# Optimization experiments

Hardware: AMD Instinct MI355X
Metric: run time of the kernel (lower is better)

## Reference

```python
import jax, jax.numpy as jnp
import numpy as np
from jax import lax

B, MID, OUT, H, W = 16, 128, 512, 112, 112
EPS = 1e-5


def _conv(x, w, stride=1, pad=0, dil=1, groups=1):
    return lax.conv_general_dilated(
        x, w, window_strides=(stride, stride),
        padding=[(pad, pad), (pad, pad)], rhs_dilation=(dil, dil),
        feature_group_count=groups,
        dimension_numbers=('NCHW', 'OIHW', 'NCHW'))


def setup_inputs() -> dict:
    key = jax.random.key(0)
    ks = jax.random.split(key, 12)
    s = 0.05
    return {
        'x': jax.random.normal(ks[0], (B, 2 * MID, H, W), jnp.float32),
        # kernel_gen: Linear(mid, mid*9, bias=False) weight [mid*9, mid]
        'W_kg': jax.random.normal(ks[1], (MID * 9, MID), jnp.float32) * s,
        # global stream: depthwise 3x3 dil=2, then 1x1 conv, BN
        'gdw_w': jax.random.normal(ks[2], (MID, 1, 3, 3), jnp.float32) * s,
        'gdw_b': jax.random.normal(ks[3], (MID,), jnp.float32) * s,
        'gpw_w': jax.random.normal(ks[4], (MID, MID, 1, 1), jnp.float32) * s,
        'gpw_b': jax.random.normal(ks[5], (MID,), jnp.float32) * s,
        'bn1_g': jnp.ones((MID,), jnp.float32),
        'bn1_b': jnp.zeros((MID,), jnp.float32),
        'bn1_m': jax.random.normal(ks[6], (MID,), jnp.float32) * s,
        'bn1_v': jax.random.uniform(ks[7], (MID,), jnp.float32, 0.5, 1.5),
        # downsample: Conv2d(2*mid, out, 3, stride=2, pad=1), BN
        'ds_w': jax.random.normal(ks[8], (OUT, 2 * MID, 3, 3), jnp.float32) * s,
        'ds_b': jax.random.normal(ks[9], (OUT,), jnp.float32) * s,
        'bn2_g': jnp.ones((OUT,), jnp.float32),
        'bn2_b': jnp.zeros((OUT,), jnp.float32),
        'bn2_m': jax.random.normal(ks[10], (OUT,), jnp.float32) * s,
        'bn2_v': jax.random.uniform(ks[11], (OUT,), jnp.float32, 0.5, 1.5),
    }


def _bn(x, g, b, m, v):  # eval-mode BatchNorm2d
    inv = g / jnp.sqrt(v + EPS)
    return x * inv[None, :, None, None] + (b - m * inv)[None, :, None, None]


def reference(x, W_kg, gdw_w, gdw_b, gpw_w, gpw_b,
              bn1_g, bn1_b, bn1_m, bn1_v,
              ds_w, ds_b, bn2_g, bn2_b, bn2_m, bn2_v):
    local_in, global_in = jnp.split(x, 2, axis=1)  # [B,MID,H,W] each
    b, c, h, w = local_in.shape

    # local branch: pool -> linear+relu kernel-gen -> per-sample depthwise 3x3
    pooled = jnp.mean(local_in, axis=(2, 3))                  # [b,c]
    kernels = jax.nn.relu(pooled @ W_kg.T)                    # [b, c*9]
    kernels = kernels.reshape(b * c, 1, 3, 3)
    local_out = _conv(local_in.reshape(1, b * c, h, w), kernels,
                      pad=1, groups=b * c).reshape(b, c, h, w)

    # global branch: depthwise dil-2 conv -> 1x1 conv -> BN -> ReLU
    g = _conv(global_in, gdw_w, pad=2, dil=2, groups=c) + gdw_b[None, :, None, None]
    g = _conv(g, gpw_w) + gpw_b[None, :, None, None]
    g = jax.nn.relu(_bn(g, bn1_g, bn1_b, bn1_m, bn1_v))

    combined = jnp.concatenate([local_out, g], axis=1)        # [b,2c,h,w]
    out = _conv(combined, ds_w, stride=2, pad=1) + ds_b[None, :, None, None]
    out = jax.nn.relu(_bn(out, bn2_g, bn2_b, bn2_m, bn2_v))   # [b,OUT,h/2,w/2]
    return out
```

## Files before the change

kernel.cpp:

```cpp
#include <hip/hip_runtime.h>


#define DEVI static __device__ __forceinline__

using bf16x8 = __attribute__((ext_vector_type(8))) short;
using f32x4  = __attribute__((ext_vector_type(4))) float;
typedef unsigned short ushort_t;

constexpr int Bn = 16, MID = 128, CHN = 256, Hh = 112, Wn = 112;
constexpr int OHn = 56, OWn = 56, OCn = 512;
constexpr int HW  = Hh * Wn;
constexpr float EPSf = 1e-5f;

constexpr size_t C_I = 56 * 64;
constexpr size_t C_P = 4 * C_I;
constexpr size_t C_H = 2 * C_P;
constexpr size_t C_B = (size_t)Hh * C_H;

DEVI ushort_t f2b(float f) {
    unsigned u = __float_as_uint(f);
    return (ushort_t)((u + 0x7FFFu + ((u >> 16) & 1u)) >> 16);
}
DEVI float b2f(ushort_t s) { return __uint_as_float(((unsigned)s) << 16); }
DEVI int pack2(float a, float b) {
    return (int)f2b(a) | ((int)f2b(b) << 16);
}

DEVI void gl_lds16(const void* g, void* l) {
    __builtin_amdgcn_global_load_lds(
        (const __attribute__((address_space(1))) unsigned int*)g,
        (__attribute__((address_space(3))) unsigned int*)l, 16, 0, 0);
}

__global__ __launch_bounds__(256) void k_wds(
        const float* __restrict__ dsw, ushort_t* __restrict__ wds2,
        const float* __restrict__ gpw_w, const float* __restrict__ gpw_b,
        const float* __restrict__ bn1g, const float* __restrict__ bn1b,
        const float* __restrict__ bn1m, const float* __restrict__ bn1v,
        const float* __restrict__ dsb,
        const float* __restrict__ bn2g, const float* __restrict__ bn2b,
        const float* __restrict__ bn2m, const float* __restrict__ bn2v,
        ushort_t* __restrict__ gpwbf,
        float* __restrict__ a1, float* __restrict__ b1,
        float* __restrict__ a2, float* __restrict__ b2,
        float* __restrict__ pooled) {
    int d = blockIdx.x * 256 + threadIdx.x;
    int j = d & 63, oc = (d >> 6) & 511, kb = d >> 15;
    int khw = kb >> 2, icc = kb & 3;
    int ph = j >> 3, c = ph ^ (oc & 7);
    int ic = icc * 64 + c * 8 + (j & 7);
    wds2[d] = f2b(dsw[((size_t)oc * CHN + ic) * 9 + khw]);
    int i = d;
    if (i < MID * MID) gpwbf[i] = f2b(gpw_w[i]);
    if (i < Bn * MID) pooled[i] = 0.f;
    if (i < OCn) {
        float inv = bn2g[i] / sqrtf(bn2v[i] + EPSf);
        a2[i] = inv;
        b2[i] = bn2b[i] + (dsb[i] - bn2m[i]) * inv;
    }
    if (i < MID) {
        float inv = bn1g[i] / sqrtf(bn1v[i] + EPSf);
        a1[i] = inv;
        b1[i] = bn1b[i] + (gpw_b[i] - bn1m[i]) * inv;
    }
}

__global__ __launch_bounds__(256) void k_kgen(const float* __restrict__ pooled,
                                              const float* __restrict__ wkg,
                                              float* __restrict__ kgen) {
    int idx = blockIdx.x * 256 + threadIdx.x;
    int b = idx / 1152, j = idx % 1152;
    int c = j & 127, tp = j >> 7;
    const float* pr = pooled + b * MID;
    const float* wr = wkg + (size_t)(c * 9 + tp) * MID;
    float s = 0.f;
#pragma unroll 8
    for (int i = 0; i < MID; i++) s += pr[i] * wr[i];
    kgen[idx] = fmaxf(s * (1.f / HW), 0.f);
}

__global__ __launch_bounds__(256) void k_xt(const float* __restrict__ x,
                                            ushort_t* __restrict__ xT,
                                            float* __restrict__ pooled) {
    __shared__ ushort_t tile[Wn * 264];
    int t = threadIdx.x;
    int bh = blockIdx.x;
    int b = bh / Hh, h = bh % Hh;
    const float* xp = x + ((size_t)b * CHN * Hh + h) * Wn;
    for (int idx = t; idx < CHN * 28; idx += 256) {
        int ch = idx / 28, q = idx % 28;
        float4 v = *(const float4*)(xp + (size_t)ch * HW + q * 4);
        int w = q * 4;
        tile[w * 264 + ch]       = f2b(v.x);
        tile[(w + 1) * 264 + ch] = f2b(v.y);
        tile[(w + 2) * 264 + ch] = f2b(v.z);
        tile[(w + 3) * 264 + ch] = f2b(v.w);
    }
    __syncthreads();
    int4* dst = (int4*)(xT + (size_t)bh * Wn * CHN);
    for (int q = t; q < Wn * CHN / 8; q += 256) {
        int w = q >> 5, c0 = (q & 31) << 3;
        dst[q] = *(const int4*)(tile + w * 264 + c0);
    }
    if (t < MID) {
        float s = 0.f;
        for (int w = 0; w < Wn; w++) s += b2f(tile[w * 264 + t]);
        atomicAdd(&pooled[b * MID + t], s);
    }
}

template <int DIL>
DEVI void dw_accum_row(const ushort_t* __restrict__ rp,
                       const float* __restrict__ wtab, int tb,
                       int c0, int wbase, float (&acc)[7][8]) {
    constexpr int NC = 7 + 2 * DIL;
    float wk[3][8];
#pragma unroll
    for (int dw = 0; dw < 3; dw++) {
        float4 lo = *(const float4*)&wtab[(tb + dw) * 128 + c0];
        float4 hi = *(const float4*)&wtab[(tb + dw) * 128 + c0 + 4];
        wk[dw][0] = lo.x; wk[dw][1] = lo.y; wk[dw][2] = lo.z; wk[dw][3] = lo.w;
        wk[dw][4] = hi.x; wk[dw][5] = hi.y; wk[dw][6] = hi.z; wk[dw][7] = hi.w;
    }
    int4 C[NC];
#pragma unroll
    for (int j = 0; j < NC; j++) {
        int w1 = wbase - DIL + j;
        int4 v = make_int4(0, 0, 0, 0);
        if ((unsigned)w1 < (unsigned)Wn)
            v = *(const int4*)(rp + (size_t)w1 * CHN);
        C[j] = v;
    }
#pragma unroll
    for (int j = 0; j < NC; j++) {
        float f[8];
        {
            unsigned u;
            u = (unsigned)C[j].x;
            f[0] = __uint_as_float(u << 16); f[1] = __uint_as_float(u & 0xffff0000u);
            u = (unsigned)C[j].y;
            f[2] = __uint_as_float(u << 16); f[3] = __uint_as_float(u & 0xffff0000u);
            u = (unsigned)C[j].z;
            f[4] = __uint_as_float(u << 16); f[5] = __uint_as_float(u & 0xffff0000u);
            u = (unsigned)C[j].w;
            f[6] = __uint_as_float(u << 16); f[7] = __uint_as_float(u & 0xffff0000u);
        }
#pragma unroll
        for (int dw = 0; dw < 3; dw++) {
            int i = j - dw * DIL;
            if (i >= 0 && i <= 6) {
#pragma unroll
                for (int k = 0; k < 8; k++) acc[i][k] += wk[dw][k] * f[k];
            }
        }
    }
}

__global__ __launch_bounds__(256, 3) void k_dw(
        const ushort_t* __restrict__ xT, const float* __restrict__ kgen,
        const float* __restrict__ gdw_w, const float* __restrict__ gdw_b,
        ushort_t* __restrict__ comb) {
    __shared__ float wtab[1152];
    int t = threadIdx.x;
    int h = blockIdx.x, by = blockIdx.y;
    int b = by >> 1, br = by & 1;
    if (br == 0) {
        const float4* src = (const float4*)(kgen + (size_t)b * 1152);
        float4* dstw = (float4*)wtab;
        dstw[t] = src[t];
        if (t < 32) dstw[256 + t] = src[256 + t];
    } else {
        for (int e4 = t; e4 < 288; e4 += 256) {
            float4 v = *(const float4*)(gdw_w + (size_t)e4 * 4);
            int e = e4 * 4;
            wtab[(e % 9) * 128 + e / 9]             = v.x;
            wtab[((e + 1) % 9) * 128 + (e + 1) / 9] = v.y;
            wtab[((e + 2) % 9) * 128 + (e + 2) / 9] = v.z;
            wtab[((e + 3) % 9) * 128 + (e + 3) / 9] = v.w;
        }
    }
    __syncthreads();
    int cg = t & 15, wl = t >> 4, c0 = cg << 3, wbase = 7 * wl;
    const ushort_t* xb = xT + (size_t)b * HW * CHN + (br ? MID : 0) + c0;
    float acc[7][8];
    if (br == 0) {
#pragma unroll
        for (int i = 0; i < 7; i++)
#pragma unroll
            for (int k = 0; k < 8; k++) acc[i][k] = 0.f;
#pragma unroll
        for (int dh = -1; dh <= 1; dh++) {
            int h1 = h + dh;
            if ((unsigned)h1 < (unsigned)Hh)
                dw_accum_row<1>(xb + (size_t)h1 * Wn * CHN, wtab,
                                (dh + 1) * 3, c0, wbase, acc);
        }
    } else {
        float4 b0 = *(const float4*)(gdw_b + c0);
        float4 b4 = *(const float4*)(gdw_b + c0 + 4);
#pragma unroll
        for (int i = 0; i < 7; i++) {
            acc[i][0] = b0.x; acc[i][1] = b0.y; acc[i][2] = b0.z; acc[i][3] = b0.w;
            acc[i][4] = b4.x; acc[i][5] = b4.y; acc[i][6] = b4.z; acc[i][7] = b4.w;
        }
#pragma unroll
        for (int dh = -1; dh <= 1; dh++) {
            int h1 = h + 2 * dh;
            if ((unsigned)h1 < (unsigned)Hh)
                dw_accum_row<2>(xb + (size_t)h1 * Wn * CHN, wtab,
                                (dh + 1) * 3, c0, wbase, acc);
        }
    }
    int gch = (br ? MID : 0) + c0;
    int icc = gch >> 6, cch = (gch & 63) >> 3;
#pragma unroll
    for (int i = 0; i < 7; i++) {
        int w = wbase + i;
        int4 O;
        O.x = pack2(acc[i][0], acc[i][1]);
        O.y = pack2(acc[i][2], acc[i][3]);
        O.z = pack2(acc[i][4], acc[i][5]);
        O.w = pack2(acc[i][6], acc[i][7]);
        int w2 = w >> 1, p = w & 1, ph = cch ^ (w2 & 7);
        *(int4*)(comb + (size_t)b * C_B + (size_t)h * C_H + p * C_P
                 + icc * C_I + w2 * 64 + ph * 8) = O;
    }
}

__global__ __launch_bounds__(256, 3) void k_pw(
        ushort_t* __restrict__ comb, const ushort_t* __restrict__ gpwbf,
        const float* __restrict__ a1, const float* __restrict__ b1) {
    __shared__ ushort_t pbuf[112 * 136];
    int t = threadIdx.x, lane = t & 63, wave = t >> 6;
    int h = blockIdx.x, b = blockIdx.y;
    const char* base = (const char*)(comb + (size_t)b * C_B + (size_t)h * C_H);
    for (int j = wave; j < 28; j += 4) {
        int s = j / 7, cc = j - s * 7;
        int p = s >> 1, ic = 2 + (s & 1);
        const char* src = base + ((size_t)p * C_P + (size_t)ic * C_I) * 2
                          + cc * 1024 + lane * 16;
        gl_lds16(src, (char*)pbuf + (size_t)s * 7168 + cc * 1024);
    }
    __syncthreads();
    int mrow = lane & 15, quad = lane >> 4;
    const short* gw = (const short*)gpwbf;
    f32x4 acc2[7][2] = {};
#pragma unroll
    for (int ks = 0; ks < 4; ks++) {
        bf16x8 bfr[2];
#pragma unroll
        for (int n = 0; n < 2; n++)
            bfr[n] = *(const bf16x8*)(gw + (size_t)(wave * 32 + n * 16 + mrow) * MID
                                         + ks * 32 + quad * 8);
        int kq = ks * 4 + quad;
#pragma unroll
        for (int m = 0; m < 7; m++) {
            int row = m * 16 + mrow;
            int p = (row >= 56) ? 1 : 0;
            int w2 = row - 56 * p;
            int slab = p * 2 + (kq >> 3);
            int ph = (kq & 7) ^ (w2 & 7);
            bf16x8 af = *(const bf16x8*)(pbuf + (size_t)slab * 3584
                                         + w2 * 64 + ph * 8);
#pragma unroll
            for (int n = 0; n < 2; n++)
                acc2[m][n] = __builtin_amdgcn_mfma_f32_16x16x32_bf16(
                    af, bfr[n], acc2[m][n], 0, 0, 0);
        }
    }
    __syncthreads();
#pragma unroll
    for (int m = 0; m < 7; m++)
#pragma unroll
        for (int n = 0; n < 2; n++) {
            int oc2 = wave * 32 + n * 16 + mrow;
            float al = a1[oc2], be = b1[oc2];
#pragma unroll
            for (int r = 0; r < 4; r++) {
                int px = m * 16 + quad * 4 + r;
                pbuf[px * 136 + oc2] = f2b(fmaxf(acc2[m][n][r] * al + be, 0.f));
            }
        }
    __syncthreads();
    int cg = t & 15, wl = t >> 4, c0 = cg << 3;
    for (int ws = 0; ws < 7; ws++) {
        int row = ws * 16 + wl;
        int p = (row >= 56) ? 1 : 0;
        int w2 = row - 56 * p;
        int4 v = *(const int4*)(pbuf + (size_t)row * 136 + c0);
        int gch = MID + c0;
        int icc = gch >> 6, cch = (gch & 63) >> 3, ph = cch ^ (w2 & 7);
        *(int4*)(comb + (size_t)b * C_B + (size_t)h * C_H + (size_t)p * C_P
                 + icc * C_I + w2 * 64 + ph * 8) = v;
    }
}

__global__ __launch_bounds__(256) void k_ds(
        const ushort_t* __restrict__ comb, const ushort_t* __restrict__ wds2,
        const float* __restrict__ a2, const float* __restrict__ b2,
        float* __restrict__ out) {
    __shared__ ushort_t lA[128 * 64];
    __shared__ ushort_t lB[128 * 64];
    int t = threadIdx.x, lane = t & 63, wave = t >> 6;
    int g = blockIdx.x;
    int xcd = g & 7, s = g >> 3;
    int octile = s & 3, pl = s >> 2;
    int pair = xcd * 56 + pl;
    int bb = pair / 28, ohp = pair % 28;
    int oh0 = ohp * 2, oc0 = octile * 128;
    int mrow = lane & 15, quad = lane >> 4;
    int wm = wave & 1, wn = wave >> 1;
    int ak = mrow & 7;

    f32x4 acc[4][4] = {};
    for (int kt = 0; kt < 36; kt++) {
        int khw = kt >> 2, icc = kt & 3;
        int kh = khw / 3, kw = khw - kh * 3;
        int p = (kw == 1) ? 0 : 1;
        bool zh0 = (oh0 == 0) && (kh == 0);
        int ldsShift = (kw == 0) ? 128 : 0;
        __syncthreads();
        if (zh0) {
            int4 z = {0, 0, 0, 0};
            *(int4*)(lB + t * 8) = z;
            *(int4*)(lB + 2048 + t * 8) = z;
        }
        if (kw == 0 && t < 16) {
            int4 z = {0, 0, 0, 0};
            *(int4*)(lB + (t >> 3) * 4096 + (t & 7) * 8) = z;
        }
        const char* asrc = (const char*)wds2
            + ((size_t)kt * 32768 + (size_t)oc0 * 64) * 2 + lane * 16;
#pragma unroll
        for (int i = 0; i < 4; i++) {
            int j = wave * 4 + i;
            gl_lds16(asrc + j * 1024, (char*)lA + j * 1024);
        }
        for (int j = wave; j < 14; j += 4) {
            int osub = (j >= 7) ? 1 : 0, jj = j - osub * 7;
            if (zh0 && osub == 0) continue;
            int r = 2 * oh0 + 2 * osub + kh - 1;
            const char* bsrc = (const char*)comb
                + ((size_t)bb * C_B + (size_t)r * C_H + (size_t)p * C_P
                   + (size_t)icc * C_I) * 2 + jj * 1024 + lane * 16;
            gl_lds16(bsrc, (char*)lB + osub * 8192 + ldsShift + jj * 1024);
        }
        __syncthreads();
        int bk = (mrow + ((kw == 0) ? 7 : 0)) & 7;
#pragma unroll
        for (int ks = 0; ks < 2; ks++) {
            bf16x8 af[4], bf[4];
#pragma unroll
            for (int m = 0; m < 4; m++) {
                int row = wm * 64 + m * 16 + mrow;
                int ph = (ks * 4 + quad) ^ ak;
                af[m] = *(const bf16x8*)(lA + row * 64 + ph * 8);
            }
#pragma unroll
            for (int n = 0; n < 4; n++) {
                int nr = wn * 64 + n * 16 + mrow;
                int ph = (ks * 4 + quad) ^ bk;
                bf[n] = *(const bf16x8*)(lB + nr * 64 + ph * 8);
            }
#pragma unroll
            for (int m = 0; m < 4; m++)
#pragma unroll
                for (int n = 0; n < 4; n++)
                    acc[m][n] = __builtin_amdgcn_mfma_f32_16x16x32_bf16(
                        af[m], bf[n], acc[m][n], 0, 0, 0);
        }
    }
#pragma unroll
    for (int m = 0; m < 4; m++) {
#pragma unroll
        for (int r4 = 0; r4 < 4; r4++) {
            int oc = oc0 + wm * 64 + m * 16 + quad * 4 + r4;
            float al = a2[oc], be = b2[oc];
#pragma unroll
            for (int n = 0; n < 4; n++) {
                int nr = wn * 64 + n * 16 + mrow;
                int osub = nr >> 6, ow = nr & 63;
                if (ow < OWn) {
                    float v = fmaxf(acc[m][n][r4] * al + be, 0.f);
                    out[((size_t)(bb * OCn + oc) * OHn + (oh0 + osub)) * OWn + ow] = v;
                }
            }
        }
    }
}

extern "C" void kernel_launch(void* const* d_in, const int* in_sizes, int n_in,
                              void* d_out, int out_size, void* d_ws, size_t ws_size,
                              hipStream_t stream) {
    const float* x     = (const float*)d_in[0];
    const float* wkg   = (const float*)d_in[1];
    const float* gdw_w = (const float*)d_in[2];
    const float* gdw_b = (const float*)d_in[3];
    const float* gpw_w = (const float*)d_in[4];
    const float* gpw_b = (const float*)d_in[5];
    const float* bn1g  = (const float*)d_in[6];
    const float* bn1b  = (const float*)d_in[7];
    const float* bn1m  = (const float*)d_in[8];
    const float* bn1v  = (const float*)d_in[9];
    const float* dsw   = (const float*)d_in[10];
    const float* dsb   = (const float*)d_in[11];
    const float* bn2g  = (const float*)d_in[12];
    const float* bn2b  = (const float*)d_in[13];
    const float* bn2m  = (const float*)d_in[14];
    const float* bn2v  = (const float*)d_in[15];

    char* ws = (char*)d_ws;
    float*    pooled = (float*)(ws + 0);
    float*    kgen   = (float*)(ws + 8192);
    float*    a1     = (float*)(ws + 81920);
    float*    b1     = (float*)(ws + 82432);
    float*    a2     = (float*)(ws + 82944);
    float*    b2     = (float*)(ws + 84992);
    ushort_t* gpwbf  = (ushort_t*)(ws + 87040);
    ushort_t* wds2   = (ushort_t*)(ws + 119808);
    ushort_t* comb   = (ushort_t*)(ws + 2479104);
    ushort_t* xT  = (ushort_t*)d_out;
    float*    out = (float*)d_out;

    k_wds <<<4608, 256, 0, stream>>>(dsw, wds2, gpw_w, gpw_b,
                                     bn1g, bn1b, bn1m, bn1v, dsb,
                                     bn2g, bn2b, bn2m, bn2v,
                                     gpwbf, a1, b1, a2, b2, pooled);
    k_xt  <<<1792, 256, 0, stream>>>(x, xT, pooled);
    k_kgen<<<72, 256, 0, stream>>>(pooled, wkg, kgen);
    k_dw  <<<dim3(Hh, Bn * 2), 256, 0, stream>>>(xT, kgen, gdw_w, gdw_b, comb);
    k_pw  <<<dim3(Hh, Bn), 256, 0, stream>>>(comb, gpwbf, a1, b1);
    k_ds  <<<1792, 256, 0, stream>>>(comb, wds2, a2, b2, out);
}
```

Baseline: 338.8 us.

## Double-buffer LDS tiles in downsample conv GEMM to overlap loads with MFMA

The stride-2 downsample convolution kernel now keeps two LDS buffers for the weight and activation tiles. It issues the global-to-LDS loads for the next K step before running MFMAs on the current one, which halves the barriers per K step and hides load latency behind compute. The cost is doubled LDS use (64KB per block), which may reduce how many blocks fit on a CU.

```diff
diff --git a/kernel.cpp b/kernel.cpp
--- a/kernel.cpp
+++ b/kernel.cpp
@@ -299,8 +299,8 @@
         const ushort_t* __restrict__ comb, const ushort_t* __restrict__ wds2,
         const float* __restrict__ a2, const float* __restrict__ b2,
         float* __restrict__ out) {
-    __shared__ ushort_t lA[128 * 64];
-    __shared__ ushort_t lB[128 * 64];
+    __shared__ __align__(16) ushort_t lA[2][128 * 64];
+    __shared__ __align__(16) ushort_t lB[2][128 * 64];
     int t = threadIdx.x, lane = t & 63, wave = t >> 6;
     int g = blockIdx.x;
     int xcd = g & 7, s = g >> 3;
@@ -312,29 +312,29 @@
     int wm = wave & 1, wn = wave >> 1;
     int ak = mrow & 7;
 
-    f32x4 acc[4][4] = {};
-    for (int kt = 0; kt < 36; kt++) {
+    auto STAGE = [&](int kt, int nb) {
         int khw = kt >> 2, icc = kt & 3;
         int kh = khw / 3, kw = khw - kh * 3;
         int p = (kw == 1) ? 0 : 1;
         bool zh0 = (oh0 == 0) && (kh == 0);
         int ldsShift = (kw == 0) ? 128 : 0;
-        __syncthreads();
+        ushort_t* A = (ushort_t*)lA[nb];
+        ushort_t* B = (ushort_t*)lB[nb];
         if (zh0) {
             int4 z = {0, 0, 0, 0};
-            *(int4*)(lB + t * 8) = z;
-            *(int4*)(lB + 2048 + t * 8) = z;
+            *(int4*)(B + t * 8) = z;
+            *(int4*)(B + 2048 + t * 8) = z;
         }
         if (kw == 0 && t < 16) {
             int4 z = {0, 0, 0, 0};
-            *(int4*)(lB + (t >> 3) * 4096 + (t & 7) * 8) = z;
+            *(int4*)(B + (t >> 3) * 4096 + (t & 7) * 8) = z;
         }
         const char* asrc = (const char*)wds2
             + ((size_t)kt * 32768 + (size_t)oc0 * 64) * 2 + lane * 16;
 #pragma unroll
         for (int i = 0; i < 4; i++) {
             int j = wave * 4 + i;
-            gl_lds16(asrc + j * 1024, (char*)lA + j * 1024);
+            gl_lds16(asrc + j * 1024, (char*)A + j * 1024);
         }
         for (int j = wave; j < 14; j += 4) {
             int osub = (j >= 7) ? 1 : 0, jj = j - osub * 7;
@@ -343,9 +343,16 @@
             const char* bsrc = (const char*)comb
                 + ((size_t)bb * C_B + (size_t)r * C_H + (size_t)p * C_P
                    + (size_t)icc * C_I) * 2 + jj * 1024 + lane * 16;
-            gl_lds16(bsrc, (char*)lB + osub * 8192 + ldsShift + jj * 1024);
-        }
-        __syncthreads();
+            gl_lds16(bsrc, (char*)B + osub * 8192 + ldsShift + jj * 1024);
+        }
+    };
+
+    f32x4 acc[4][4] = {};
+
+    auto COMPUTE = [&](int kt, int nb) {
+        const ushort_t* A = (const ushort_t*)lA[nb];
+        const ushort_t* B = (const ushort_t*)lB[nb];
+        int khw = kt >> 2, kh = khw / 3, kw = khw - kh * 3;
         int bk = (mrow + ((kw == 0) ? 7 : 0)) & 7;
 #pragma unroll
         for (int ks = 0; ks < 2; ks++) {
@@ -354,13 +361,13 @@
             for (int m = 0; m < 4; m++) {
                 int row = wm * 64 + m * 16 + mrow;
                 int ph = (ks * 4 + quad) ^ ak;
-                af[m] = *(const bf16x8*)(lA + row * 64 + ph * 8);
+                af[m] = *(const bf16x8*)(A + row * 64 + ph * 8);
             }
 #pragma unroll
             for (int n = 0; n < 4; n++) {
                 int nr = wn * 64 + n * 16 + mrow;
                 int ph = (ks * 4 + quad) ^ bk;
-                bf[n] = *(const bf16x8*)(lB + nr * 64 + ph * 8);
+                bf[n] = *(const bf16x8*)(B + nr * 64 + ph * 8);
             }
 #pragma unroll
             for (int m = 0; m < 4; m++)
@@ -369,6 +376,17 @@
                     acc[m][n] = __builtin_amdgcn_mfma_f32_16x16x32_bf16(
                         af[m], bf[n], acc[m][n], 0, 0, 0);
         }
+    };
+
+    STAGE(0, 0);
+    __syncthreads();
+    for (int kt0 = 0; kt0 < 36; kt0 += 2) {
+        STAGE(kt0 + 1, 1);
+        COMPUTE(kt0, 0);
+        __syncthreads();
+        if (kt0 + 2 < 36) STAGE(kt0 + 2, 0);
+        COMPUTE(kt0 + 1, 1);
+        if (kt0 + 2 < 36) __syncthreads();
     }
 #pragma unroll
     for (int m = 0; m < 4; m++) {
```

Result: slower. 391.8 us (+15.7%).

## Reuse odd-column B tile for kw=0 and kw=2 taps in downsample conv

Applied to the files above, without the earlier changes.

The stride-2 downsample GEMM loop is reorganized so that the kw=0 and kw=2 taps, which read the same odd-column plane of the combined activation, share a single B staging into LDS. The B rows are then read at a one-row offset, and two weight tiles are staged into separate LDS buffers. This cuts B global loads and barrier rounds from 36 to 24 per block, at the cost of extra LDS (48KB) and a possible drop in occupancy.

```diff
diff --git a/kernel.cpp b/kernel.cpp
--- a/kernel.cpp
+++ b/kernel.cpp
@@ -299,8 +299,10 @@
         const ushort_t* __restrict__ comb, const ushort_t* __restrict__ wds2,
         const float* __restrict__ a2, const float* __restrict__ b2,
         float* __restrict__ out) {
-    __shared__ ushort_t lA[128 * 64];
-    __shared__ ushort_t lB[128 * 64];
+    __shared__ __align__(16) ushort_t lds[3 * 8192];
+    ushort_t* lB  = lds;
+    ushort_t* lA0 = lds + 8192;
+    ushort_t* lA1 = lds + 16384;
     int t = threadIdx.x, lane = t & 63, wave = t >> 6;
     int g = blockIdx.x;
     int xcd = g & 7, s = g >> 3;
@@ -312,30 +314,16 @@
     int wm = wave & 1, wn = wave >> 1;
     int ak = mrow & 7;
 
-    f32x4 acc[4][4] = {};
-    for (int kt = 0; kt < 36; kt++) {
-        int khw = kt >> 2, icc = kt & 3;
-        int kh = khw / 3, kw = khw - kh * 3;
-        int p = (kw == 1) ? 0 : 1;
-        bool zh0 = (oh0 == 0) && (kh == 0);
-        int ldsShift = (kw == 0) ? 128 : 0;
-        __syncthreads();
-        if (zh0) {
-            int4 z = {0, 0, 0, 0};
-            *(int4*)(lB + t * 8) = z;
-            *(int4*)(lB + 2048 + t * 8) = z;
-        }
-        if (kw == 0 && t < 16) {
-            int4 z = {0, 0, 0, 0};
-            *(int4*)(lB + (t >> 3) * 4096 + (t & 7) * 8) = z;
-        }
+    auto stageA = [&](int kt, ushort_t* A) {
         const char* asrc = (const char*)wds2
             + ((size_t)kt * 32768 + (size_t)oc0 * 64) * 2 + lane * 16;
 #pragma unroll
         for (int i = 0; i < 4; i++) {
             int j = wave * 4 + i;
-            gl_lds16(asrc + j * 1024, (char*)lA + j * 1024);
-        }
+            gl_lds16(asrc + j * 1024, (char*)A + j * 1024);
+        }
+    };
+    auto stageB = [&](int kh, int icc, int p, int shiftB, bool zh0) {
         for (int j = wave; j < 14; j += 4) {
             int osub = (j >= 7) ? 1 : 0, jj = j - osub * 7;
             if (zh0 && osub == 0) continue;
@@ -343,10 +331,13 @@
             const char* bsrc = (const char*)comb
                 + ((size_t)bb * C_B + (size_t)r * C_H + (size_t)p * C_P
                    + (size_t)icc * C_I) * 2 + jj * 1024 + lane * 16;
-            gl_lds16(bsrc, (char*)lB + osub * 8192 + ldsShift + jj * 1024);
-        }
-        __syncthreads();
-        int bk = (mrow + ((kw == 0) ? 7 : 0)) & 7;
+            gl_lds16(bsrc, (char*)lB + osub * 8192 + shiftB + jj * 1024);
+        }
+    };
+
+    f32x4 acc[4][4] = {};
+
+    auto mfmaStep = [&](const ushort_t* A, int rowOff, int bk) {
 #pragma unroll
         for (int ks = 0; ks < 2; ks++) {
             bf16x8 af[4], bf[4];
@@ -354,11 +345,11 @@
             for (int m = 0; m < 4; m++) {
                 int row = wm * 64 + m * 16 + mrow;
                 int ph = (ks * 4 + quad) ^ ak;
-                af[m] = *(const bf16x8*)(lA + row * 64 + ph * 8);
+                af[m] = *(const bf16x8*)(A + row * 64 + ph * 8);
             }
 #pragma unroll
             for (int n = 0; n < 4; n++) {
-                int nr = wn * 64 + n * 16 + mrow;
+                int nr = wn * 64 + n * 16 + mrow + rowOff;
                 int ph = (ks * 4 + quad) ^ bk;
                 bf[n] = *(const bf16x8*)(lB + nr * 64 + ph * 8);
             }
@@ -368,6 +359,36 @@
                 for (int n = 0; n < 4; n++)
                     acc[m][n] = __builtin_amdgcn_mfma_f32_16x16x32_bf16(
                         af[m], bf[n], acc[m][n], 0, 0, 0);
+        }
+    };
+
+    for (int ss = 0; ss < 24; ss++) {
+        int kh = ss >> 3, sub = ss & 7;
+        bool isPair = sub < 4;
+        int icc = isPair ? sub : sub - 4;
+        bool zh0 = (oh0 == 0) && (kh == 0);
+        __syncthreads();
+        if (zh0) {
+            int4 z = {0, 0, 0, 0};
+            *(int4*)(lB + t * 8) = z;
+            *(int4*)(lB + 2048 + t * 8) = z;
+        }
+        if (isPair) {
+            if (t < 16) {
+                int4 z = {0, 0, 0, 0};
+                *(int4*)(lB + (t >> 3) * 4096 + (t & 7) * 8) = z;
+            }
+            stageA((kh * 3 + 0) * 4 + icc, lA0);
+            stageA((kh * 3 + 2) * 4 + icc, lA1);
+            stageB(kh, icc, 1, 128, zh0);
+            __syncthreads();
+            mfmaStep(lA0, 0, (mrow + 7) & 7);
+            mfmaStep(lA1, 1, mrow & 7);
+        } else {
+            stageA((kh * 3 + 1) * 4 + icc, lA0);
+            stageB(kh, icc, 0, 0, zh0);
+            __syncthreads();
+            mfmaStep(lA0, 0, mrow & 7);
         }
     }
 #pragma unroll
```

After: 360.3 us. 1.06x slower.
